# Kernel tuning notes

Measured on AMD Instinct MI355X. Metric: run time of the kernel, lower is better.

## Reference

```python
import jax, jax.numpy as jnp
import numpy as np

N = 100000
C_IN = 256
C_OUT = 256
LN_EPS = 1e-5


def setup_inputs() -> dict:
    key = jax.random.key(0)
    ks = jax.random.split(key, 6)
    x = jax.random.normal(ks[0], (N, C_IN), dtype=jnp.float32)
    idx1 = jax.random.randint(ks[1], (N,), 0, N, dtype=jnp.int64 if jax.config.jax_enable_x64 else jnp.int32)
    idx2 = jax.random.randint(ks[2], (N,), 0, N, dtype=idx1.dtype)
    idx3 = jax.random.randint(ks[3], (N,), 0, N, dtype=idx1.dtype)
    idx4 = jax.random.randint(ks[4], (N,), 0, N, dtype=idx1.dtype)
    W = jax.random.normal(ks[5], (5 * C_IN, C_OUT), dtype=jnp.float32) * (1.0 / np.sqrt(5 * C_IN))
    b = jnp.zeros((C_OUT,), dtype=jnp.float32)
    gamma = jnp.ones((C_OUT,), dtype=jnp.float32)
    beta = jnp.zeros((C_OUT,), dtype=jnp.float32)
    return {"x": x, "idx1": idx1, "idx2": idx2, "idx3": idx3, "idx4": idx4,
            "W": W, "b": b, "gamma": gamma, "beta": beta}


def reference(x, idx1, idx2, idx3, idx4, W, b, gamma, beta):
    # Four sparse-mm neighbor gathers (one nonzero of value 1 per row)
    a = x[idx1]
    bb = x[idx2]
    c = x[idx3]
    d = x[idx4]
    # symmetric combine + concat -> [N, 5*C_IN]
    patch = jnp.concatenate([x, jnp.abs(a - c), a + c, jnp.abs(bb - d), bb + d], axis=-1)
    y = patch @ W + b
    # LayerNorm over channels
    mu = jnp.mean(y, axis=-1, keepdims=True)
    var = jnp.mean(jnp.square(y - mu), axis=-1, keepdims=True)
    y = (y - mu) * jax.lax.rsqrt(var + LN_EPS) * gamma + beta
    # residual (in_channels == out_channels -> identity projection)
    y = y + x
    # torch nn.GELU default is exact (erf) gelu
    return jax.nn.gelu(y, approximate=False)
```

## Files before the change

### kernel.cpp

```cpp
#include <hip/hip_runtime.h>


#define N_ROWS   100000
#define C        256
#define BK       64
#define NCHUNK   20
#define BM       64
#define LN_EPS   1e-5f
#define APAD     72

typedef __bf16 bf16;
typedef bf16  bf16x8 __attribute__((ext_vector_type(8)));
typedef float f32x4  __attribute__((ext_vector_type(4)));

union BV { bf16x8 v; bf16 h[8]; };
union FV { float4 q[4]; float f[16]; };

__global__ void wprep(const float* __restrict__ W, bf16* __restrict__ Wt) {
    int t = blockIdx.x * 256 + threadIdx.x;
    if (t >= NCHUNK * C * BK) return;
    int kc  = t / (C * BK);
    int rem = t - kc * (C * BK);
    int n   = rem >> 6;
    int kk  = rem & 63;
    Wt[t] = (bf16)W[(size_t)(kc * BK + kk) * C + n];
}

__global__ __launch_bounds__(256, 3)
void fused(const float* __restrict__ x,
           const int* __restrict__ idx1, const int* __restrict__ idx2,
           const int* __restrict__ idx3, const int* __restrict__ idx4,
           const bf16* __restrict__ Wt,
           const float* __restrict__ bias,
           const float* __restrict__ gamma_, const float* __restrict__ beta_,
           float* __restrict__ out)
{
    __shared__ __align__(16) bf16 Alds[BM * APAD];
    __shared__ __align__(16) bf16 Wlds[C * APAD];
    __shared__ int   gidx[4][BM];
    __shared__ float redsum[BM][4];
    __shared__ float redsq [BM][4];
    __shared__ float s_mu[BM], s_rs[BM];

    const int tid  = threadIdx.x;
    const int lane = tid & 63;
    const int wv   = tid >> 6;
    const int quad = lane >> 4;
    const int l16  = lane & 15;
    const int r0   = blockIdx.x * BM;

    {
        int which = tid >> 6;
        int r     = tid & 63;
        int gr    = r0 + r; if (gr >= N_ROWS) gr = 0;
        const int* ip = (which == 0) ? idx1 : (which == 1) ? idx2
                      : (which == 2) ? idx3 : idx4;
        gidx[which][r] = ip[gr];
    }

    f32x4 acc[4][4] = {};

    const int r_st = tid >> 2;
    const int q_st = tid & 3;
    int gr_self = r0 + r_st; if (gr_self >= N_ROWS) gr_self = 0;

    for (int kc = 0; kc < NCHUNK; ++kc) {
        __syncthreads();

        {
            const int seg = kc >> 2;
            const int off = ((kc & 3) << 6) + (q_st << 4);
            FV u;
            if (seg == 0) {
                const float4* p = (const float4*)(x + (size_t)gr_self * C + off);
                #pragma unroll
                for (int j = 0; j < 4; ++j) u.q[j] = p[j];
            } else {
                const int ia = (seg <= 2) ? gidx[0][r_st] : gidx[1][r_st];
                const int ic = (seg <= 2) ? gidx[2][r_st] : gidx[3][r_st];
                const bool sab = (seg & 1);
                const float4* pa = (const float4*)(x + (size_t)ia * C + off);
                const float4* pc = (const float4*)(x + (size_t)ic * C + off);
                FV ua, uc;
                #pragma unroll
                for (int j = 0; j < 4; ++j) { ua.q[j] = pa[j]; uc.q[j] = pc[j]; }
                #pragma unroll
                for (int j = 0; j < 16; ++j)
                    u.f[j] = sab ? fabsf(ua.f[j] - uc.f[j]) : (ua.f[j] + uc.f[j]);
            }
            BV b0, b1;
            #pragma unroll
            for (int j = 0; j < 8; ++j) { b0.h[j] = (bf16)u.f[j]; b1.h[j] = (bf16)u.f[j + 8]; }
            bf16x8* dst = (bf16x8*)&Alds[r_st * APAD + (q_st << 4)];
            dst[0] = b0.v; dst[1] = b1.v;
        }

        {
            const bf16x8* src = (const bf16x8*)(Wt + (size_t)kc * (C * BK));
            #pragma unroll
            for (int j = 0; j < 8; ++j) {
                int g = tid + j * 256;
                bf16x8 w = src[g];
                *(bf16x8*)&Wlds[(g >> 3) * APAD + ((g & 7) << 3)] = w;
            }
        }
        __syncthreads();

        #pragma unroll
        for (int ks = 0; ks < 2; ++ks) {
            const int kb = ks * 32 + quad * 8;
            bf16x8 af[4], bfr[4];
            #pragma unroll
            for (int mi = 0; mi < 4; ++mi)
                af[mi] = *(const bf16x8*)&Alds[(mi * 16 + l16) * APAD + kb];
            #pragma unroll
            for (int ni = 0; ni < 4; ++ni)
                bfr[ni] = *(const bf16x8*)&Wlds[(wv * 64 + ni * 16 + l16) * APAD + kb];
            #pragma unroll
            for (int mi = 0; mi < 4; ++mi)
                #pragma unroll
                for (int ni = 0; ni < 4; ++ni)
                    acc[mi][ni] = __builtin_amdgcn_mfma_f32_16x16x32_bf16(
                        af[mi], bfr[ni], acc[mi][ni], 0, 0, 0);
        }
    }

    float bcol[4], gcol[4], ecol[4];
    #pragma unroll
    for (int ni = 0; ni < 4; ++ni) {
        int cidx = wv * 64 + ni * 16 + l16;
        bcol[ni] = bias[cidx]; gcol[ni] = gamma_[cidx]; ecol[ni] = beta_[cidx];
    }
    #pragma unroll
    for (int mi = 0; mi < 4; ++mi)
        #pragma unroll
        for (int ni = 0; ni < 4; ++ni)
            #pragma unroll
            for (int rg = 0; rg < 4; ++rg)
                acc[mi][ni][rg] += bcol[ni];

    #pragma unroll
    for (int mi = 0; mi < 4; ++mi) {
        #pragma unroll
        for (int rg = 0; rg < 4; ++rg) {
            float s = 0.f, q = 0.f;
            #pragma unroll
            for (int ni = 0; ni < 4; ++ni) {
                float y = acc[mi][ni][rg];
                s += y; q += y * y;
            }
            #pragma unroll
            for (int m = 1; m <= 8; m <<= 1) {
                s += __shfl_xor(s, m, 64);
                q += __shfl_xor(q, m, 64);
            }
            if (l16 == 0) {
                int row = mi * 16 + quad * 4 + rg;
                redsum[row][wv] = s;
                redsq [row][wv] = q;
            }
        }
    }
    __syncthreads();
    if (tid < BM) {
        float s  = redsum[tid][0] + redsum[tid][1] + redsum[tid][2] + redsum[tid][3];
        float q  = redsq [tid][0] + redsq [tid][1] + redsq [tid][2] + redsq [tid][3];
        float mu = s * (1.0f / C);
        float var = q * (1.0f / C) - mu * mu;
        s_mu[tid] = mu;
        s_rs[tid] = rsqrtf(var + LN_EPS);
    }
    __syncthreads();

    #pragma unroll
    for (int mi = 0; mi < 4; ++mi) {
        #pragma unroll
        for (int rg = 0; rg < 4; ++rg) {
            int row  = mi * 16 + quad * 4 + rg;
            int grow = r0 + row;
            if (grow >= N_ROWS) continue;
            float mu = s_mu[row], rs = s_rs[row];
            #pragma unroll
            for (int ni = 0; ni < 4; ++ni) {
                int cidx = wv * 64 + ni * 16 + l16;
                float y = (acc[mi][ni][rg] - mu) * rs * gcol[ni] + ecol[ni];
                y += x[(size_t)grow * C + cidx];
                float g = 0.5f * y * (1.0f + erff(y * 0.70710678118654752f));
                out[(size_t)grow * C + cidx] = g;
            }
        }
    }
}

extern "C" void kernel_launch(void* const* d_in, const int* in_sizes, int n_in,
                              void* d_out, int out_size, void* d_ws, size_t ws_size,
                              hipStream_t stream) {
    const float* x  = (const float*)d_in[0];
    const int*   i1 = (const int*)d_in[1];
    const int*   i2 = (const int*)d_in[2];
    const int*   i3 = (const int*)d_in[3];
    const int*   i4 = (const int*)d_in[4];
    const float* W  = (const float*)d_in[5];
    const float* b  = (const float*)d_in[6];
    const float* gm = (const float*)d_in[7];
    const float* bt = (const float*)d_in[8];
    float* outp = (float*)d_out;
    bf16* Wt = (bf16*)d_ws;

    wprep<<<(NCHUNK * C * BK + 255) / 256, 256, 0, stream>>>(W, Wt);
    fused<<<(N_ROWS + BM - 1) / BM, 256, 0, stream>>>(
        x, i1, i2, i3, i4, Wt, b, gm, bt, outp);
}
```

Before: 397.1 us.

## Prefetch next A chunk in registers, async-load W to LDS, swizzle LDS layout

Loads the next K-chunk's gathered rows into registers while the MFMAs for the current chunk run, so global gather latency overlaps compute. The weight chunk goes straight into LDS with global_load_lds instead of a register round trip. Padded LDS is replaced by an XOR-swizzled layout, with W pre-swizzled and K-reordered in wprep so |a-c| and a+c come from one gather, halving x gathers. Smaller LDS allows 4 blocks per SM, at the cost of more register pressure from the staging registers.

Measured after the change: 424.2 us. 1.07x slower.

```diff
diff --git a/kernel.cpp b/kernel.cpp
--- a/kernel.cpp
+++ b/kernel.cpp
@@ -7,7 +7,6 @@
 #define NCHUNK   20
 #define BM       64
 #define LN_EPS   1e-5f
-#define APAD     72
 
 typedef __bf16 bf16;
 typedef bf16  bf16x8 __attribute__((ext_vector_type(8)));
@@ -16,17 +15,28 @@
 union BV { bf16x8 v; bf16 h[8]; };
 union FV { float4 q[4]; float f[16]; };
 
+__device__ __forceinline__ void async_g2l(const void* g, void* l) {
+    __builtin_amdgcn_global_load_lds(
+        (const __attribute__((address_space(1))) void*)g,
+        (__attribute__((address_space(3))) void*)l, 16, 0, 0);
+}
+
 __global__ void wprep(const float* __restrict__ W, bf16* __restrict__ Wt) {
     int t = blockIdx.x * 256 + threadIdx.x;
-    if (t >= NCHUNK * C * BK) return;
-    int kc  = t / (C * BK);
-    int rem = t - kc * (C * BK);
-    int n   = rem >> 6;
-    int kk  = rem & 63;
-    Wt[t] = (bf16)W[(size_t)(kc * BK + kk) * C + n];
-}
-
-__global__ __launch_bounds__(256, 3)
+    if (t >= NCHUNK * BK * C) return;
+    int n  = t & 255;
+    int r  = t >> 8;
+    int kc = r >> 6;
+    int kk = r & 63;
+    int kRow;
+    if (kc < 4)       kRow = kc * 64 + kk;
+    else if (kc < 12) { int u = kc - 4;  kRow = 256 + (u & 1) * 256 + (u >> 1) * 64 + kk; }
+    else              { int u = kc - 12; kRow = 768 + (u & 1) * 256 + (u >> 1) * 64 + kk; }
+    int gs = (kk >> 3) ^ (n & 7);
+    Wt[(size_t)kc * (C * BK) + n * 64 + gs * 8 + (kk & 7)] = (bf16)W[(size_t)kRow * C + n];
+}
+
+__global__ __launch_bounds__(256, 4)
 void fused(const float* __restrict__ x,
            const int* __restrict__ idx1, const int* __restrict__ idx2,
            const int* __restrict__ idx3, const int* __restrict__ idx4,
@@ -35,12 +45,11 @@
            const float* __restrict__ gamma_, const float* __restrict__ beta_,
            float* __restrict__ out)
 {
-    __shared__ __align__(16) bf16 Alds[BM * APAD];
-    __shared__ __align__(16) bf16 Wlds[C * APAD];
-    __shared__ int   gidx[4][BM];
-    __shared__ float redsum[BM][4];
-    __shared__ float redsq [BM][4];
-    __shared__ float s_mu[BM], s_rs[BM];
+    __shared__ __align__(16) bf16 Wl[C * BK];
+    __shared__ __align__(16) union {
+        bf16 a[BM * BK];
+        struct { float rsum[BM][4]; float rsq[BM][4]; float mu[BM]; float rs[BM]; } red;
+    } SA;
 
     const int tid  = threadIdx.x;
     const int lane = tid & 63;
@@ -49,73 +58,80 @@
     const int l16  = lane & 15;
     const int r0   = blockIdx.x * BM;
 
-    {
-        int which = tid >> 6;
-        int r     = tid & 63;
-        int gr    = r0 + r; if (gr >= N_ROWS) gr = 0;
-        const int* ip = (which == 0) ? idx1 : (which == 1) ? idx2
-                      : (which == 2) ? idx3 : idx4;
-        gidx[which][r] = ip[gr];
-    }
-
-    f32x4 acc[4][4] = {};
-
     const int r_st = tid >> 2;
     const int q_st = tid & 3;
     int gr_self = r0 + r_st; if (gr_self >= N_ROWS) gr_self = 0;
+    const int ia = idx1[gr_self], ib = idx2[gr_self];
+    const int ic = idx3[gr_self], id = idx4[gr_self];
+
+    f32x4 acc[4][4] = {};
+    bf16x8 st0, st1;
+    bf16x8 h0, h1;
+
+    {
+        const float4* p = (const float4*)(x + (size_t)gr_self * C + (q_st << 4));
+        FV u;
+        #pragma unroll
+        for (int j = 0; j < 4; ++j) u.q[j] = p[j];
+        BV b0, b1;
+        #pragma unroll
+        for (int j = 0; j < 8; ++j) { b0.h[j] = (bf16)u.f[j]; b1.h[j] = (bf16)u.f[j + 8]; }
+        st0 = b0.v; st1 = b1.v;
+    }
 
     for (int kc = 0; kc < NCHUNK; ++kc) {
+        {
+            int g0 = (2 * q_st)     ^ (r_st & 7);
+            int g1 = (2 * q_st + 1) ^ (r_st & 7);
+            *(bf16x8*)&SA.a[r_st * 64 + g0 * 8] = st0;
+            *(bf16x8*)&SA.a[r_st * 64 + g1 * 8] = st1;
+        }
+        {
+            const bf16* wsrc = Wt + (size_t)kc * (C * BK);
+            #pragma unroll
+            for (int j = 0; j < 8; ++j) {
+                int g = j * 256 + tid;
+                async_g2l(wsrc + g * 8, &Wl[g * 8]);
+            }
+        }
         __syncthreads();
 
-        {
-            const int seg = kc >> 2;
-            const int off = ((kc & 3) << 6) + (q_st << 4);
-            FV u;
-            if (seg == 0) {
-                const float4* p = (const float4*)(x + (size_t)gr_self * C + off);
+        const int kn = kc + 1;
+        FV la, lc;
+        int mode = 0;
+        if (kn < 4) {
+            mode = 1;
+            const float4* p = (const float4*)(x + (size_t)gr_self * C + (kn << 6) + (q_st << 4));
+            #pragma unroll
+            for (int j = 0; j < 4; ++j) la.q[j] = p[j];
+        } else if (kn < NCHUNK) {
+            int u = (kn < 12) ? (kn - 4) : (kn - 12);
+            if ((u & 1) == 0) {
+                mode = 2;
+                int rA = (kn < 12) ? ia : ib;
+                int rC = (kn < 12) ? ic : id;
+                int off = ((u >> 1) << 6) + (q_st << 4);
+                const float4* pa = (const float4*)(x + (size_t)rA * C + off);
+                const float4* pc = (const float4*)(x + (size_t)rC * C + off);
                 #pragma unroll
-                for (int j = 0; j < 4; ++j) u.q[j] = p[j];
-            } else {
-                const int ia = (seg <= 2) ? gidx[0][r_st] : gidx[1][r_st];
-                const int ic = (seg <= 2) ? gidx[2][r_st] : gidx[3][r_st];
-                const bool sab = (seg & 1);
-                const float4* pa = (const float4*)(x + (size_t)ia * C + off);
-                const float4* pc = (const float4*)(x + (size_t)ic * C + off);
-                FV ua, uc;
-                #pragma unroll
-                for (int j = 0; j < 4; ++j) { ua.q[j] = pa[j]; uc.q[j] = pc[j]; }
-                #pragma unroll
-                for (int j = 0; j < 16; ++j)
-                    u.f[j] = sab ? fabsf(ua.f[j] - uc.f[j]) : (ua.f[j] + uc.f[j]);
-            }
-            BV b0, b1;
-            #pragma unroll
-            for (int j = 0; j < 8; ++j) { b0.h[j] = (bf16)u.f[j]; b1.h[j] = (bf16)u.f[j + 8]; }
-            bf16x8* dst = (bf16x8*)&Alds[r_st * APAD + (q_st << 4)];
-            dst[0] = b0.v; dst[1] = b1.v;
-        }
-
-        {
-            const bf16x8* src = (const bf16x8*)(Wt + (size_t)kc * (C * BK));
-            #pragma unroll
-            for (int j = 0; j < 8; ++j) {
-                int g = tid + j * 256;
-                bf16x8 w = src[g];
-                *(bf16x8*)&Wlds[(g >> 3) * APAD + ((g & 7) << 3)] = w;
-            }
-        }
-        __syncthreads();
+                for (int j = 0; j < 4; ++j) { la.q[j] = pa[j]; lc.q[j] = pc[j]; }
+            }
+        }
 
         #pragma unroll
         for (int ks = 0; ks < 2; ++ks) {
-            const int kb = ks * 32 + quad * 8;
+            const int gbase = ks * 4 + quad;
             bf16x8 af[4], bfr[4];
             #pragma unroll
-            for (int mi = 0; mi < 4; ++mi)
-                af[mi] = *(const bf16x8*)&Alds[(mi * 16 + l16) * APAD + kb];
-            #pragma unroll
-            for (int ni = 0; ni < 4; ++ni)
-                bfr[ni] = *(const bf16x8*)&Wlds[(wv * 64 + ni * 16 + l16) * APAD + kb];
+            for (int mi = 0; mi < 4; ++mi) {
+                int m = mi * 16 + l16;
+                af[mi] = *(const bf16x8*)&SA.a[m * 64 + ((gbase ^ (m & 7)) * 8)];
+            }
+            #pragma unroll
+            for (int ni = 0; ni < 4; ++ni) {
+                int n = wv * 64 + ni * 16 + l16;
+                bfr[ni] = *(const bf16x8*)&Wl[n * 64 + ((gbase ^ (n & 7)) * 8)];
+            }
             #pragma unroll
             for (int mi = 0; mi < 4; ++mi)
                 #pragma unroll
@@ -123,6 +139,26 @@
                     acc[mi][ni] = __builtin_amdgcn_mfma_f32_16x16x32_bf16(
                         af[mi], bfr[ni], acc[mi][ni], 0, 0, 0);
         }
+
+        if (mode == 1) {
+            BV b0, b1;
+            #pragma unroll
+            for (int j = 0; j < 8; ++j) { b0.h[j] = (bf16)la.f[j]; b1.h[j] = (bf16)la.f[j + 8]; }
+            st0 = b0.v; st1 = b1.v;
+        } else if (mode == 2) {
+            BV d0, d1, s0, s1;
+            #pragma unroll
+            for (int j = 0; j < 8; ++j) {
+                d0.h[j] = (bf16)fabsf(la.f[j]     - lc.f[j]);
+                d1.h[j] = (bf16)fabsf(la.f[j + 8] - lc.f[j + 8]);
+                s0.h[j] = (bf16)(la.f[j]     + lc.f[j]);
+                s1.h[j] = (bf16)(la.f[j + 8] + lc.f[j + 8]);
+            }
+            st0 = d0.v; st1 = d1.v; h0 = s0.v; h1 = s1.v;
+        } else if (kn < NCHUNK) {
+            st0 = h0; st1 = h1;
+        }
+        __syncthreads();
     }
 
     float bcol[4], gcol[4], ecol[4];
@@ -156,19 +192,19 @@
             }
             if (l16 == 0) {
                 int row = mi * 16 + quad * 4 + rg;
-                redsum[row][wv] = s;
-                redsq [row][wv] = q;
+                SA.red.rsum[row][wv] = s;
+                SA.red.rsq [row][wv] = q;
             }
         }
     }
     __syncthreads();
     if (tid < BM) {
-        float s  = redsum[tid][0] + redsum[tid][1] + redsum[tid][2] + redsum[tid][3];
-        float q  = redsq [tid][0] + redsq [tid][1] + redsq [tid][2] + redsq [tid][3];
+        float s  = SA.red.rsum[tid][0] + SA.red.rsum[tid][1] + SA.red.rsum[tid][2] + SA.red.rsum[tid][3];
+        float q  = SA.red.rsq [tid][0] + SA.red.rsq [tid][1] + SA.red.rsq [tid][2] + SA.red.rsq [tid][3];
         float mu = s * (1.0f / C);
         float var = q * (1.0f / C) - mu * mu;
-        s_mu[tid] = mu;
-        s_rs[tid] = rsqrtf(var + LN_EPS);
+        SA.red.mu[tid] = mu;
+        SA.red.rs[tid] = rsqrtf(var + LN_EPS);
     }
     __syncthreads();
 
@@ -179,7 +215,7 @@
             int row  = mi * 16 + quad * 4 + rg;
             int grow = r0 + row;
             if (grow >= N_ROWS) continue;
-            float mu = s_mu[row], rs = s_rs[row];
+            float mu = SA.red.mu[row], rs = SA.red.rs[row];
             #pragma unroll
             for (int ni = 0; ni < 4; ++ni) {
                 int cidx = wv * 64 + ni * 16 + l16;
@@ -207,7 +243,7 @@
     float* outp = (float*)d_out;
     bf16* Wt = (bf16*)d_ws;
 
-    wprep<<<(NCHUNK * C * BK + 255) / 256, 256, 0, stream>>>(W, Wt);
+    wprep<<<(NCHUNK * BK * C + 255) / 256, 256, 0, stream>>>(W, Wt);
     fused<<<(N_ROWS + BM - 1) / BM, 256, 0, stream>>>(
         x, i1, i2, i3, i4, Wt, b, gm, bt, outp);
 }
```
